# Kernel optimization log

Measured on AMD Instinct MI355X. Metric: run time of the kernel, lower is better.

The kernel has to match this reference:

```python
import jax, jax.numpy as jnp
import numpy as np

HID, INTER, DK = 768, 1536, 128
NEG_INF = 1.0e12
LOG512 = float(np.log(512.0))


def setup_inputs() -> dict:
    key = jax.random.key(0)
    k1, k2, k3 = jax.random.split(key, 3)
    B, S = 4, 2048
    hidden_states = jax.random.normal(k1, (B, S, HID), dtype=jnp.float32)
    attention_mask = jnp.ones((B, S), dtype=jnp.int32)
    # i_dense: hidden -> 2*INTER + DK (no bias); o_dense: INTER -> hidden (no bias)
    Wi = jax.random.normal(k2, (HID, 2 * INTER + DK), dtype=jnp.float32) * (HID ** -0.5)
    Wo = jax.random.normal(k3, (INTER, HID), dtype=jnp.float32) * (INTER ** -0.5)
    q_gamma = jnp.ones((DK,), dtype=jnp.float32)  # ScaleOffset scale, offset=False
    k_gamma = jnp.ones((DK,), dtype=jnp.float32)
    return {"hidden_states": hidden_states, "Wi": Wi, "Wo": Wo,
            "q_gamma": q_gamma, "k_gamma": k_gamma,
            "attention_mask": attention_mask}


def reference(hidden_states, Wi, Wo, q_gamma, k_gamma, attention_mask):
    # i_dense + swish, then split into u, v, qk
    x = jax.nn.silu(jnp.einsum('bsh,ho->bso', hidden_states, Wi))
    u = x[..., :INTER]
    v = x[..., INTER:2 * INTER]
    qk = x[..., 2 * INTER:]
    q = qk * q_gamma
    k = qk * k_gamma
    # single-head attention scores
    a = jnp.einsum('bmd,bnd->bmn', q, k) / (DK ** 0.5)
    mask = attention_mask[:, None, :]  # [B,1,N]
    a = jnp.where(mask == 0, -NEG_INF, a)
    l = jnp.sum(attention_mask, axis=-1, keepdims=True)[:, :, None].astype(a.dtype)  # [B,1,1]
    # softmax_plus: softmax(a * log(l) / log(512))
    A = jax.nn.softmax(a * jnp.log(l) / LOG512, axis=-1)
    # dropout inactive in eval mode
    o = jnp.einsum('bmi,ih->bmh', u * jnp.einsum('bmn,bnd->bmd', A, v), Wo)
    return o
```

## Files before the change

### kernel.cpp

```cpp
#include <hip/hip_runtime.h>
#include <hip/hip_bf16.h>
#include <math.h>

#define BATCH 4
#define SEQ   2048
#define HID   768
#define INTER 1536
#define DK    128
#define NTOT  3200
#define NTOTP 3328
#define MROWS 8192
#define LN512 6.2383246250395075f

typedef _Float16 half8   __attribute__((ext_vector_type(8)));
typedef _Float16 half4   __attribute__((ext_vector_type(4)));
typedef float    floatx4 __attribute__((ext_vector_type(4)));
typedef float    floatx16 __attribute__((ext_vector_type(16)));

typedef const __attribute__((address_space(1))) unsigned int* gas1_t;
typedef __attribute__((address_space(3))) unsigned int* las3_t;

static __device__ __forceinline__ void load16(const _Float16* g, _Float16* l) {
    __builtin_amdgcn_global_load_lds((gas1_t)g, (las3_t)l, 16, 0, 0);
}
#define WAIT_VM(N)    asm volatile("s_waitcnt vmcnt(" #N ")" ::: "memory")
#define WAIT_LGKM0()  asm volatile("s_waitcnt lgkmcnt(0)" ::: "memory")
#define BARRIER_RAW() asm volatile("s_barrier" ::: "memory")

__global__ __launch_bounds__(256) void prep_kernel(
    const float* __restrict__ H, _Float16* __restrict__ Hb,
    const float* __restrict__ Wi, _Float16* __restrict__ WiT,
    const float* __restrict__ Wo, _Float16* __restrict__ WoT,
    const int* __restrict__ mask, float* __restrict__ scales)
{
    __shared__ _Float16 tile[32][33];
    __shared__ int sh[256];
    const int bid = blockIdx.x, tid = threadIdx.x;
    if (bid < 3072) {
        const int i = (bid * 256 + tid) * 8;
        float4 a = *reinterpret_cast<const float4*>(H + i);
        float4 b = *reinterpret_cast<const float4*>(H + i + 4);
        half8 h = {(_Float16)a.x, (_Float16)a.y, (_Float16)a.z, (_Float16)a.w,
                   (_Float16)b.x, (_Float16)b.y, (_Float16)b.z, (_Float16)b.w};
        *reinterpret_cast<half8*>(Hb + i) = h;
    } else if (bid < 3072 + 2496) {
        const int l = bid - 3072;
        const int c0 = (l % 104) * 32, r0 = (l / 104) * 32;
        const int tx = tid & 31, ty = tid >> 5;
#pragma unroll
        for (int j = 0; j < 32; j += 8)
            tile[tx][ty + j] = (c0 + tx < NTOT)
                ? (_Float16)Wi[(size_t)(r0 + ty + j) * NTOT + c0 + tx]
                : (_Float16)0.0f;
        __syncthreads();
#pragma unroll
        for (int j = 0; j < 32; j += 8)
            WiT[(size_t)(c0 + ty + j) * HID + r0 + tx] = tile[ty + j][tx];
    } else if (bid < 3072 + 2496 + 1152) {
        const int l = bid - (3072 + 2496);
        const int c0 = (l % 24) * 32, r0 = (l / 24) * 32;
        const int tx = tid & 31, ty = tid >> 5;
#pragma unroll
        for (int j = 0; j < 32; j += 8)
            tile[tx][ty + j] = (_Float16)Wo[(size_t)(r0 + ty + j) * HID + c0 + tx];
        __syncthreads();
#pragma unroll
        for (int j = 0; j < 32; j += 8)
            WoT[(size_t)(c0 + ty + j) * INTER + r0 + tx] = tile[ty + j][tx];
    } else {
        const int b = bid - (3072 + 2496 + 1152);
        int s = 0;
        for (int i = tid; i < SEQ; i += 256) s += mask[b * SEQ + i];
        sh[tid] = s;
        __syncthreads();
        for (int off = 128; off > 0; off >>= 1) {
            if (tid < off) sh[tid] += sh[tid + off];
            __syncthreads();
        }
        if (tid == 0) scales[b] = logf((float)sh[0]) / LN512;
    }
}

struct TileCtx {
    int tid, wave, lane, quad, l16, l31, half, wm, wn, c0, c1;
};
static __device__ __forceinline__ TileCtx make_ctx() {
    TileCtx t;
    t.tid = threadIdx.x;
    t.wave = t.tid >> 6; t.lane = t.tid & 63;
    t.quad = t.lane >> 4; t.l16 = t.lane & 15;
    t.l31 = t.lane & 31;  t.half = t.lane >> 5;
    t.wm = (t.wave & 1) * 64;
    t.wn = (t.wave >> 1) * 64;
    t.c0 = t.tid;
    t.c1 = t.tid + 256;
    return t;
}

static __device__ __forceinline__ void gemm_mainloop_3s32(
    const TileCtx& t,
    const _Float16* __restrict__ Ag, int lda,
    const _Float16* __restrict__ Bg, int ldb,
    int K, _Float16* smem, floatx16 acc[2][2])
{
    const int r0i = t.c0 >> 2, s0 = (((r0i >> 1) ^ (r0i >> 3)) & 3);
    const int r1i = t.c1 >> 2, s1 = (((r1i >> 1) ^ (r1i >> 3)) & 3);
    const int ak0 = ((t.c0 & 3) ^ s0) * 8;
    const int ak1 = ((t.c1 & 3) ^ s1) * 8;
    const _Float16* a0 = Ag + (size_t)r0i * lda + ak0;
    const _Float16* a1 = Ag + (size_t)r1i * lda + ak1;
    const _Float16* b0 = Bg + (size_t)r0i * ldb + ak0;
    const _Float16* b1 = Bg + (size_t)r1i * ldb + ak1;
    _Float16* Asl = smem + t.c0 * 8;
    _Float16* Bsl = smem + 12288 + t.c0 * 8;
    const int nIter = K >> 5;

    const int fsw = ((t.l31 >> 1) ^ (t.l31 >> 3)) & 3;

    load16(a0, Asl);        load16(a1, Asl + 2048);
    load16(b0, Bsl);        load16(b1, Bsl + 2048);
    if (nIter > 1) {
        load16(a0 + 32, Asl + 4096); load16(a1 + 32, Asl + 6144);
        load16(b0 + 32, Bsl + 4096); load16(b1 + 32, Bsl + 6144);
    }

    int sc = 0, sp = 2;
    for (int k = 0; k < nIter; ++k) {
        if (k + 1 < nIter) { WAIT_VM(4); } else { WAIT_VM(0); }
        BARRIER_RAW();
        if (k + 2 < nIter) {
            const int off = sp * 4096;
            const int k0 = (k + 2) << 5;
            load16(a0 + k0, Asl + off); load16(a1 + k0, Asl + off + 2048);
            load16(b0 + k0, Bsl + off); load16(b1 + k0, Bsl + off + 2048);
        }
        const _Float16* Ab = smem + sc * 4096;
        const _Float16* Bb = smem + 12288 + sc * 4096;
        half8 af[2][2], bf[2][2];
#pragma unroll
        for (int mt = 0; mt < 2; ++mt)
#pragma unroll
            for (int h = 0; h < 2; ++h)
                af[mt][h] = *reinterpret_cast<const half8*>(
                    Ab + (t.wm + mt * 32 + t.l31) * 32 + (((h * 2 + t.half) ^ fsw) * 8));
#pragma unroll
        for (int nt = 0; nt < 2; ++nt)
#pragma unroll
            for (int h = 0; h < 2; ++h)
                bf[nt][h] = *reinterpret_cast<const half8*>(
                    Bb + (t.wn + nt * 32 + t.l31) * 32 + (((h * 2 + t.half) ^ fsw) * 8));
#pragma unroll
        for (int h = 0; h < 2; ++h)
#pragma unroll
            for (int mt = 0; mt < 2; ++mt)
#pragma unroll
                for (int nt = 0; nt < 2; ++nt)
                    acc[mt][nt] = __builtin_amdgcn_mfma_f32_32x32x16_f16(af[mt][h], bf[nt][h], acc[mt][nt], 0, 0, 0);
        WAIT_LGKM0();
        sc = (sc == 2) ? 0 : sc + 1;
        sp = (sp == 2) ? 0 : sp + 1;
    }
}

__global__ __launch_bounds__(512, 2) void gemm1_kernel(
    const _Float16* __restrict__ Hb, const _Float16* __restrict__ WiT,
    const float* __restrict__ qg, const float* __restrict__ kg,
    _Float16* __restrict__ u, _Float16* __restrict__ vT,
    _Float16* __restrict__ q, _Float16* __restrict__ k)
{
    __shared__ _Float16 smem[65536];
    const int tid = threadIdx.x;
    const int lane = tid & 63, wave = tid >> 6;
    const int quad = lane >> 4, l16 = lane & 15;
    const int wm = wave >> 2, wn = wave & 3;

    const int f = blockIdx.x;
    const int xcd = f & 7, i = f >> 3;
    const int m0 = (xcd * 4 + (i & 3)) * 256;
    const int ntile = i >> 2;
    const int n0 = ntile * 256;

    const _Float16* Ag = Hb  + (size_t)m0 * HID;
    const _Float16* Bg = WiT + (size_t)n0 * HID;

    const int rA = tid >> 2;
    const int csw = ((tid & 3) ^ ((rA >> 1) & 3)) * 8;
    const _Float16* pa0 = Ag + (size_t)rA * HID + csw;
    const _Float16* pa1 = pa0 + (size_t)128 * HID;
    const _Float16* pb0 = Bg + (size_t)rA * HID + csw;
    const _Float16* pb1 = pb0 + (size_t)128 * HID;

    const int sw8 = (l16 >> 1) & 3;
    const int qs  = (quad ^ sw8) * 8;
    const int aoff = (wm * 128 + l16) * 32 + qs;
    const int boff = 8192 + (wn * 64 + l16) * 32 + qs;

    floatx4 acc[8][4] = {};

    const int nKt = HID / 32;

#pragma unroll
    for (int pt = 0; pt < 3; ++pt) {
        _Float16* ld = smem + pt * 16384 + tid * 8;
        const int ko = pt * 32;
        load16(pa0 + ko, ld);
        load16(pa1 + ko, ld + 4096);
        load16(pb0 + ko, ld + 8192);
        load16(pb1 + ko, ld + 12288);
    }
    WAIT_VM(8);
    BARRIER_RAW();

    for (int t = 0; t < nKt; ++t) {
        const _Float16* sl = smem + (t & 3) * 16384;
        if (t + 3 < nKt) {
            _Float16* ld = smem + ((t + 3) & 3) * 16384 + tid * 8;
            const int ko = (t + 3) * 32;
            load16(pa0 + ko, ld);        load16(pa1 + ko, ld + 4096);
            load16(pb0 + ko, ld + 8192); load16(pb1 + ko, ld + 12288);
        }
        half8 af[8], bf[4];
#pragma unroll
        for (int mt = 0; mt < 8; ++mt)
            af[mt] = *reinterpret_cast<const half8*>(sl + aoff + mt * 512);
#pragma unroll
        for (int nt = 0; nt < 4; ++nt)
            bf[nt] = *reinterpret_cast<const half8*>(sl + boff + nt * 512);
        __builtin_amdgcn_s_setprio(1);
#pragma unroll
        for (int mt = 0; mt < 8; ++mt)
#pragma unroll
            for (int nt = 0; nt < 4; ++nt)
                acc[mt][nt] = __builtin_amdgcn_mfma_f32_16x16x32_f16(af[mt], bf[nt], acc[mt][nt], 0, 0, 0);
        __builtin_amdgcn_s_setprio(0);
        if (t <= nKt - 4)      { WAIT_VM(8); }
        else if (t == nKt - 3) { WAIT_VM(4); }
        else if (t == nKt - 2) { WAIT_VM(0); }
        BARRIER_RAW();
    }
    __syncthreads();

    if (ntile < 6) {
#pragma unroll
        for (int mt = 0; mt < 8; ++mt) {
#pragma unroll
            for (int nt = 0; nt < 4; ++nt) {
                const int col = n0 + wn * 64 + nt * 16 + l16;
#pragma unroll
                for (int i2 = 0; i2 < 4; ++i2) {
                    const int row = m0 + wm * 128 + mt * 16 + quad * 4 + i2;
                    float x = acc[mt][nt][i2];
                    float y = x / (1.0f + __expf(-x));
                    u[(size_t)row * INTER + col] = (_Float16)y;
                }
            }
        }
    } else if (ntile < 12) {
        const int bb = m0 >> 11, sloc = m0 & (SEQ - 1), cI = n0 - INTER;
#pragma unroll
        for (int mt = 0; mt < 8; ++mt) {
#pragma unroll
            for (int nt = 0; nt < 4; ++nt) {
                const int cl  = wn * 64 + nt * 16 + l16;
                const int rl0 = wm * 128 + mt * 16 + quad * 4;
                half4 pk;
#pragma unroll
                for (int i2 = 0; i2 < 4; ++i2) {
                    float x = acc[mt][nt][i2];
                    pk[i2] = (_Float16)(x / (1.0f + __expf(-x)));
                }
                *reinterpret_cast<half4*>(smem + cl * 256 + (rl0 ^ ((cl & 31) << 3))) = pk;
            }
        }
        __syncthreads();
#pragma unroll
        for (int p = 0; p < 16; ++p) {
            const int chunk = p * 512 + tid;
            const int cl = chunk >> 5, scn = chunk & 31;
            half8 v = *reinterpret_cast<const half8*>(smem + cl * 256 + ((scn ^ (cl & 31)) << 3));
            *reinterpret_cast<half8*>(vT + ((size_t)bb * INTER + cI + cl) * SEQ + sloc + scn * 8) = v;
        }
    } else {
        if (wn < 2) {
#pragma unroll
            for (int mt = 0; mt < 8; ++mt) {
#pragma unroll
                for (int nt = 0; nt < 4; ++nt) {
                    const int cq = wn * 64 + nt * 16 + l16;
                    const float qgv = qg[cq], kgv = kg[cq];
#pragma unroll
                    for (int i2 = 0; i2 < 4; ++i2) {
                        const int row = m0 + wm * 128 + mt * 16 + quad * 4 + i2;
                        float x = acc[mt][nt][i2];
                        float y = x / (1.0f + __expf(-x));
                        q[(size_t)row * DK + cq] = (_Float16)(y * qgv);
                        k[(size_t)row * DK + cq] = (_Float16)(y * kgv);
                    }
                }
            }
        }
    }
}

__global__ __launch_bounds__(256) void scores_kernel(
    const _Float16* __restrict__ q, const _Float16* __restrict__ k,
    const int* __restrict__ mask, const float* __restrict__ scales,
    _Float16* __restrict__ P)
{
    __shared__ _Float16 ps[16 * 2056];
    __shared__ float redmax[4][16];
    __shared__ float redsum[4][16];
    const int f = blockIdx.x;
    const int xcd = f & 7, i = f >> 3;
    const int b = xcd >> 1;
    const int m0 = ((xcd & 1) * 64 + i) * 16;
    const int tid = threadIdx.x;
    const int wave = tid >> 6, lane = tid & 63, quad = lane >> 4, l16 = lane & 15;
    const float scale = scales[b];

    half8 aq[4];
    const _Float16* qrow = q + (b * SEQ + m0 + l16) * DK + quad * 8;
#pragma unroll
    for (int kk = 0; kk < 4; ++kk) aq[kk] = *reinterpret_cast<const half8*>(qrow + kk * 32);

    floatx4 sc[32];
#pragma unroll
    for (int nt = 0; nt < 32; ++nt) {
        int n0 = nt * 64 + wave * 16;
        const _Float16* krow = k + (b * SEQ + n0 + l16) * DK + quad * 8;
        floatx4 acc = {};
#pragma unroll
        for (int kk = 0; kk < 4; ++kk) {
            half8 bq = *reinterpret_cast<const half8*>(krow + kk * 32);
            acc = __builtin_amdgcn_mfma_f32_16x16x32_f16(aq[kk], bq, acc, 0, 0, 0);
        }
        sc[nt] = acc;
    }

    const float rs = 0.08838834764831845f * scale;
    const float mval = -1e12f * scale;
    float rmax[4] = {-3.4e38f, -3.4e38f, -3.4e38f, -3.4e38f};
#pragma unroll
    for (int nt = 0; nt < 32; ++nt) {
        int ncol = nt * 64 + wave * 16 + l16;
        bool mok = mask[b * SEQ + ncol] != 0;
#pragma unroll
        for (int i2 = 0; i2 < 4; ++i2) {
            float s = mok ? sc[nt][i2] * rs : mval;
            sc[nt][i2] = s;
            rmax[i2] = fmaxf(rmax[i2], s);
        }
    }
#pragma unroll
    for (int i2 = 0; i2 < 4; ++i2) {
#pragma unroll
        for (int off = 1; off < 16; off <<= 1)
            rmax[i2] = fmaxf(rmax[i2], __shfl_xor(rmax[i2], off, 64));
    }
    if (l16 == 0) {
#pragma unroll
        for (int i2 = 0; i2 < 4; ++i2) redmax[wave][quad * 4 + i2] = rmax[i2];
    }
    __syncthreads();
#pragma unroll
    for (int i2 = 0; i2 < 4; ++i2) {
        int r = quad * 4 + i2;
        rmax[i2] = fmaxf(fmaxf(redmax[0][r], redmax[1][r]), fmaxf(redmax[2][r], redmax[3][r]));
    }
    float rsum[4] = {0.f, 0.f, 0.f, 0.f};
#pragma unroll
    for (int nt = 0; nt < 32; ++nt) {
#pragma unroll
        for (int i2 = 0; i2 < 4; ++i2) {
            float e = __expf(sc[nt][i2] - rmax[i2]);
            sc[nt][i2] = e;
            rsum[i2] += e;
        }
    }
#pragma unroll
    for (int i2 = 0; i2 < 4; ++i2) {
#pragma unroll
        for (int off = 1; off < 16; off <<= 1) rsum[i2] += __shfl_xor(rsum[i2], off, 64);
    }
    if (l16 == 0) {
#pragma unroll
        for (int i2 = 0; i2 < 4; ++i2) redsum[wave][quad * 4 + i2] = rsum[i2];
    }
    __syncthreads();
#pragma unroll
    for (int i2 = 0; i2 < 4; ++i2) {
        int r = quad * 4 + i2;
        float tot = redsum[0][r] + redsum[1][r] + redsum[2][r] + redsum[3][r];
        float inv = 1.0f / tot;
#pragma unroll
        for (int nt = 0; nt < 32; ++nt) {
            int ncol = nt * 64 + wave * 16 + l16;
            ps[r * 2056 + ncol] = (_Float16)(sc[nt][i2] * inv);
        }
    }
    __syncthreads();
    _Float16* Pb = P + ((size_t)b * SEQ + m0) * SEQ;
#pragma unroll
    for (int p = 0; p < 16; ++p) {
        const int chunk = p * 256 + tid;
        const int row = chunk >> 8, c8 = chunk & 255;
        half8 v = *reinterpret_cast<const half8*>(ps + row * 2056 + c8 * 8);
        *reinterpret_cast<half8*>(Pb + (size_t)row * SEQ + c8 * 8) = v;
    }
}

__global__ __launch_bounds__(256) void pv_kernel(
    const _Float16* __restrict__ P, const _Float16* __restrict__ vT,
    _Float16* __restrict__ u)
{
    __shared__ _Float16 smem[24576];
    TileCtx t = make_ctx();
    const int f = blockIdx.x;
    const int xcd = f & 7, i = f >> 3;
    const int b = i / 24, j = i % 24;
    const int m0 = (xcd * 2 + (j & 1)) * 128;
    const int n0 = (j >> 1) * 128;
    const _Float16* Pb  = P  + (size_t)b * SEQ * SEQ;
    const _Float16* vTb = vT + (size_t)b * INTER * SEQ;

    floatx16 acc[2][2] = {};
    gemm_mainloop_3s32(t, Pb + (size_t)m0 * SEQ, SEQ, vTb + (size_t)n0 * SEQ, SEQ, SEQ, smem, acc);

#pragma unroll
    for (int mt = 0; mt < 2; ++mt) {
#pragma unroll
        for (int nt = 0; nt < 2; ++nt) {
            int col = n0 + t.wn + nt * 32 + t.l31;
#pragma unroll
            for (int reg = 0; reg < 16; ++reg) {
                int row = m0 + t.wm + mt * 32 + (reg & 3) + 8 * (reg >> 2) + 4 * t.half;
                size_t gidx = ((size_t)(b * SEQ + row)) * INTER + col;
                float uv = (float)u[gidx];
                u[gidx] = (_Float16)(acc[mt][nt][reg] * uv);
            }
        }
    }
}

__global__ __launch_bounds__(256) void gemm2_kernel(
    const _Float16* __restrict__ tin, const _Float16* __restrict__ WoT,
    float* __restrict__ out)
{
    __shared__ _Float16 smem[24576];
    TileCtx t = make_ctx();
    const int f = blockIdx.x;
    const int xcd = f & 7, i = f >> 3;
    const int m0 = ((xcd << 3) | (i & 7)) * 128;
    const int n0 = (i >> 3) * 128;

    floatx16 acc[2][2] = {};
    gemm_mainloop_3s32(t, tin + (size_t)m0 * INTER, INTER, WoT + (size_t)n0 * INTER, INTER, INTER, smem, acc);

#pragma unroll
    for (int mt = 0; mt < 2; ++mt) {
#pragma unroll
        for (int nt = 0; nt < 2; ++nt) {
            int col = n0 + t.wn + nt * 32 + t.l31;
#pragma unroll
            for (int reg = 0; reg < 16; ++reg) {
                int row = m0 + t.wm + mt * 32 + (reg & 3) + 8 * (reg >> 2) + 4 * t.half;
                out[(size_t)row * HID + col] = acc[mt][nt][reg];
            }
        }
    }
}

extern "C" void kernel_launch(void* const* d_in, const int* in_sizes, int n_in,
                              void* d_out, int out_size, void* d_ws, size_t ws_size,
                              hipStream_t stream) {
    const float* H    = (const float*)d_in[0];
    const float* Wi   = (const float*)d_in[1];
    const float* Wo   = (const float*)d_in[2];
    const float* qg   = (const float*)d_in[3];
    const float* kg   = (const float*)d_in[4];
    const int*   mask = (const int*)d_in[5];
    float* out = (float*)d_out;

    char* base = (char*)d_ws;
    size_t off = 0;
    auto alloc = [&](size_t bytes) { void* p = base + off; off = (off + bytes + 255) & ~(size_t)255; return p; };
    _Float16* Hb   = (_Float16*)alloc((size_t)MROWS * HID * 2);
    _Float16* WiT  = (_Float16*)alloc((size_t)NTOTP * HID * 2);
    _Float16* WoT  = (_Float16*)alloc((size_t)HID * INTER * 2);
    _Float16* u    = (_Float16*)alloc((size_t)MROWS * INTER * 2);
    _Float16* vT   = (_Float16*)alloc((size_t)BATCH * INTER * SEQ * 2);
    _Float16* q    = (_Float16*)alloc((size_t)MROWS * DK * 2);
    _Float16* k    = (_Float16*)alloc((size_t)MROWS * DK * 2);
    _Float16* P    = (_Float16*)alloc((size_t)BATCH * SEQ * SEQ * 2);
    float*    scales = (float*)alloc(4 * sizeof(float));

    prep_kernel<<<6724, 256, 0, stream>>>(H, Hb, Wi, WiT, Wo, WoT, mask, scales);
    gemm1_kernel<<<416, 512, 0, stream>>>(Hb, WiT, qg, kg, u, vT, q, k);
    scores_kernel<<<512, 256, 0, stream>>>(q, k, mask, scales, P);
    pv_kernel<<<768, 256, 0, stream>>>(P, vT, u);
    gemm2_kernel<<<384, 256, 0, stream>>>(u, WoT, out);
}
```

Before: 296.5 us.

## Store P in fragment-ordered layout and stream A fragments directly to registers in PV

The softmax kernel now writes P in a blocked layout with 8-element column chunks interleaved across rows, so each MFMA A-fragment is one contiguous 16-byte global load. The PV kernel loads its P operand straight into registers with double-buffered fragments and keeps only the V^T tile in LDS with a 3-stage ring, which halves shared memory. This removes the LDS staging and LDS reads for the P operand, at the cost of hand-tuned vmcnt waits and more register pressure. The global reads of P are also less coalesced across rows.

Measured after the change: 293.1 us. Within noise of the previous version (-1.1%).

```diff
diff --git a/kernel.cpp b/kernel.cpp
--- a/kernel.cpp
+++ b/kernel.cpp
@@ -26,6 +26,8 @@
 #define WAIT_VM(N)    asm volatile("s_waitcnt vmcnt(" #N ")" ::: "memory")
 #define WAIT_LGKM0()  asm volatile("s_waitcnt lgkmcnt(0)" ::: "memory")
 #define BARRIER_RAW() asm volatile("s_barrier" ::: "memory")
+#define GLOAD16(dst, ptr) \
+    asm volatile("global_load_dwordx4 %0, %1, off" : "=v"(dst) : "v"(ptr) : "memory")
 
 __global__ __launch_bounds__(256) void prep_kernel(
     const float* __restrict__ H, _Float16* __restrict__ Hb,
@@ -399,32 +401,101 @@
         }
     }
     __syncthreads();
-    _Float16* Pb = P + ((size_t)b * SEQ + m0) * SEQ;
+    _Float16* Pfb = P + (size_t)b * SEQ * SEQ;
 #pragma unroll
     for (int p = 0; p < 16; ++p) {
         const int chunk = p * 256 + tid;
-        const int row = chunk >> 8, c8 = chunk & 255;
+        const int row = chunk & 15, c8 = chunk >> 4;
         half8 v = *reinterpret_cast<const half8*>(ps + row * 2056 + c8 * 8);
-        *reinterpret_cast<half8*>(Pb + (size_t)row * SEQ + c8 * 8) = v;
-    }
+        *reinterpret_cast<half8*>(Pfb + ((size_t)c8 * SEQ + m0 + row) * 8) = v;
+    }
+}
+
+static __device__ __forceinline__ void pv_iter(
+    const TileCtx& t, int k, _Float16* smem,
+    const _Float16* b0, const _Float16* b1,
+    const _Float16* pA0, const _Float16* pA1,
+    half8 (&afc)[2][2], half8 (&afn)[2][2],
+    floatx16 acc[2][2], int fsw)
+{
+    const _Float16* Bb = smem + (k % 3) * 4096;
+    half8 bf[2][2];
+#pragma unroll
+    for (int nt = 0; nt < 2; ++nt)
+#pragma unroll
+        for (int h = 0; h < 2; ++h)
+            bf[nt][h] = *reinterpret_cast<const half8*>(
+                Bb + (t.wn + nt * 32 + t.l31) * 32 + (((h * 2 + t.half) ^ fsw) * 8));
+    if (k + 1 < 64) {
+        const size_t co = (size_t)(k + 1) * 4 * (SEQ * 8);
+        GLOAD16(afn[0][0], pA0 + co);
+        GLOAD16(afn[0][1], pA0 + co + 2 * (SEQ * 8));
+        GLOAD16(afn[1][0], pA1 + co);
+        GLOAD16(afn[1][1], pA1 + co + 2 * (SEQ * 8));
+    }
+    if (k + 2 < 64) {
+        _Float16* ld = smem + ((k + 2) % 3) * 4096 + t.c0 * 8;
+        const int ko = (k + 2) * 32;
+        load16(b0 + ko, ld);
+        load16(b1 + ko, ld + 2048);
+    }
+    if (k <= 61)      { WAIT_VM(6); }
+    else if (k == 62) { WAIT_VM(4); }
+    else              { WAIT_VM(0); }
+    __builtin_amdgcn_sched_barrier(0);
+    __builtin_amdgcn_s_setprio(1);
+#pragma unroll
+    for (int h = 0; h < 2; ++h)
+#pragma unroll
+        for (int mt = 0; mt < 2; ++mt)
+#pragma unroll
+            for (int nt = 0; nt < 2; ++nt)
+                acc[mt][nt] = __builtin_amdgcn_mfma_f32_32x32x16_f16(afc[mt][h], bf[nt][h], acc[mt][nt], 0, 0, 0);
+    __builtin_amdgcn_s_setprio(0);
+    BARRIER_RAW();
 }
 
 __global__ __launch_bounds__(256) void pv_kernel(
-    const _Float16* __restrict__ P, const _Float16* __restrict__ vT,
+    const _Float16* __restrict__ Pf, const _Float16* __restrict__ vT,
     _Float16* __restrict__ u)
 {
-    __shared__ _Float16 smem[24576];
+    __shared__ _Float16 smem[12288];
     TileCtx t = make_ctx();
     const int f = blockIdx.x;
     const int xcd = f & 7, i = f >> 3;
     const int b = i / 24, j = i % 24;
     const int m0 = (xcd * 2 + (j & 1)) * 128;
     const int n0 = (j >> 1) * 128;
-    const _Float16* Pb  = P  + (size_t)b * SEQ * SEQ;
+    const _Float16* Pfb = Pf + (size_t)b * SEQ * SEQ;
     const _Float16* vTb = vT + (size_t)b * INTER * SEQ;
 
+    const int r0i = t.c0 >> 2, s0 = (((r0i >> 1) ^ (r0i >> 3)) & 3);
+    const int r1i = t.c1 >> 2, s1 = (((r1i >> 1) ^ (r1i >> 3)) & 3);
+    const _Float16* b0 = vTb + (size_t)(n0 + r0i) * SEQ + ((t.c0 & 3) ^ s0) * 8;
+    const _Float16* b1 = vTb + (size_t)(n0 + r1i) * SEQ + ((t.c1 & 3) ^ s1) * 8;
+    _Float16* Bsl = smem + t.c0 * 8;
+    const int fsw = ((t.l31 >> 1) ^ (t.l31 >> 3)) & 3;
+
+    const _Float16* pA0 = Pfb + (size_t)t.half * (SEQ * 8)
+                        + (size_t)(m0 + t.wm + t.l31) * 8;
+    const _Float16* pA1 = pA0 + 32 * 8;
+
     floatx16 acc[2][2] = {};
-    gemm_mainloop_3s32(t, Pb + (size_t)m0 * SEQ, SEQ, vTb + (size_t)n0 * SEQ, SEQ, SEQ, smem, acc);
+    half8 afA[2][2], afB[2][2];
+
+    load16(b0, Bsl);        load16(b1, Bsl + 2048);
+    load16(b0 + 32, Bsl + 4096); load16(b1 + 32, Bsl + 6144);
+    GLOAD16(afA[0][0], pA0);
+    GLOAD16(afA[0][1], pA0 + 2 * (SEQ * 8));
+    GLOAD16(afA[1][0], pA1);
+    GLOAD16(afA[1][1], pA1 + 2 * (SEQ * 8));
+    WAIT_VM(4);
+    BARRIER_RAW();
+
+    for (int k = 0; k < 64; k += 2) {
+        pv_iter(t, k,     smem, b0, b1, pA0, pA1, afA, afB, acc, fsw);
+        pv_iter(t, k + 1, smem, b0, b1, pA0, pA1, afB, afA, acc, fsw);
+    }
 
 #pragma unroll
     for (int mt = 0; mt < 2; ++mt) {
```

## Register double-buffer fragments across GEMMs and load P directly in MFMA layout

Applied to the files above, without the earlier changes.

Reworks the GEMM main loops in gemm1, gemm2 and pv so LDS fragment reads for the next k-step are issued before the MFMAs of the current step, with ping-pong register buffers, a 4-slot LDS ring, and one barrier per iteration. The softmax kernel now writes P in a fragment-friendly interleaved layout ([k/8][row][8]). This lets pv_kernel read its A operand straight from global memory into registers via inline global_load_dwordx4, skipping LDS for P. The goal is to hide LDS latency and cut barrier and LDS traffic. The cost is higher register pressure and hand-tuned vmcnt waits, which could break if the load counts change.

Result: no change. 298.0 us (+0.5%).

```diff
diff --git a/kernel.cpp b/kernel.cpp
--- a/kernel.cpp
+++ b/kernel.cpp
@@ -26,6 +26,8 @@
 #define WAIT_VM(N)    asm volatile("s_waitcnt vmcnt(" #N ")" ::: "memory")
 #define WAIT_LGKM0()  asm volatile("s_waitcnt lgkmcnt(0)" ::: "memory")
 #define BARRIER_RAW() asm volatile("s_barrier" ::: "memory")
+#define GLOAD16(dst, ptr) \
+    asm volatile("global_load_dwordx4 %0, %1, off" : "=v"(dst) : "v"(ptr) : "memory")
 
 __global__ __launch_bounds__(256) void prep_kernel(
     const float* __restrict__ H, _Float16* __restrict__ Hb,
@@ -97,7 +99,56 @@
     return t;
 }
 
-static __device__ __forceinline__ void gemm_mainloop_3s32(
+#define RO32_READ(FR, SLOT) do {                                               \
+    const _Float16* Ab_ = smem + (SLOT) * 8192;                                \
+    const _Float16* Bb_ = Ab_ + 4096;                                          \
+    _Pragma("unroll")                                                          \
+    for (int mt = 0; mt < 2; ++mt)                                             \
+        _Pragma("unroll")                                                      \
+        for (int h = 0; h < 2; ++h)                                            \
+            FR##a[mt][h] = *reinterpret_cast<const half8*>(                    \
+                Ab_ + (t.wm + mt * 32 + t.l31) * 32 + (((h * 2 + t.half) ^ fsw) * 8)); \
+    _Pragma("unroll")                                                          \
+    for (int nt = 0; nt < 2; ++nt)                                             \
+        _Pragma("unroll")                                                      \
+        for (int h = 0; h < 2; ++h)                                            \
+            FR##b[nt][h] = *reinterpret_cast<const half8*>(                    \
+                Bb_ + (t.wn + nt * 32 + t.l31) * 32 + (((h * 2 + t.half) ^ fsw) * 8)); \
+} while (0)
+
+#define RO32_MMA(FR) do {                                                      \
+    __builtin_amdgcn_s_setprio(1);                                             \
+    _Pragma("unroll")                                                          \
+    for (int h = 0; h < 2; ++h)                                                \
+        _Pragma("unroll")                                                      \
+        for (int mt = 0; mt < 2; ++mt)                                         \
+            _Pragma("unroll")                                                  \
+            for (int nt = 0; nt < 2; ++nt)                                     \
+                acc[mt][nt] = __builtin_amdgcn_mfma_f32_32x32x16_f16(          \
+                    FR##a[mt][h], FR##b[nt][h], acc[mt][nt], 0, 0, 0);         \
+    __builtin_amdgcn_s_setprio(0);                                             \
+} while (0)
+
+#define RO32_STAGE(K) do {                                                     \
+    _Float16* ld_ = smem2 + ((K) & 3) * 8192 + t.c0 * 8;                       \
+    const int ko_ = (K) << 5;                                                  \
+    load16(a0 + ko_, ld_);        load16(a1 + ko_, ld_ + 2048);                \
+    load16(b0 + ko_, ld_ + 4096); load16(b1 + ko_, ld_ + 6144);                \
+} while (0)
+
+#define RO32_ITER(K, CUR, NXT) do {                                            \
+    if ((K) + 2 < nIter) RO32_STAGE((K) + 2);                                  \
+    if ((K) + 2 < nIter)      { WAIT_VM(4); }                                  \
+    else if ((K) + 1 < nIter) { WAIT_VM(0); }                                  \
+    else                      { WAIT_VM(0); }                                  \
+    __builtin_amdgcn_sched_barrier(0);                                         \
+    BARRIER_RAW();                                                             \
+    if ((K) + 1 < nIter) RO32_READ(NXT, ((K) + 1) & 3);                        \
+    RO32_MMA(CUR);                                                             \
+    WAIT_LGKM0();                                                              \
+} while (0)
+
+static __device__ __forceinline__ void gemm_mainloop_ro32(
     const TileCtx& t,
     const _Float16* __restrict__ Ag, int lda,
     const _Float16* __restrict__ Bg, int ldb,
@@ -105,60 +156,25 @@
 {
     const int r0i = t.c0 >> 2, s0 = (((r0i >> 1) ^ (r0i >> 3)) & 3);
     const int r1i = t.c1 >> 2, s1 = (((r1i >> 1) ^ (r1i >> 3)) & 3);
-    const int ak0 = ((t.c0 & 3) ^ s0) * 8;
-    const int ak1 = ((t.c1 & 3) ^ s1) * 8;
-    const _Float16* a0 = Ag + (size_t)r0i * lda + ak0;
-    const _Float16* a1 = Ag + (size_t)r1i * lda + ak1;
-    const _Float16* b0 = Bg + (size_t)r0i * ldb + ak0;
-    const _Float16* b1 = Bg + (size_t)r1i * ldb + ak1;
-    _Float16* Asl = smem + t.c0 * 8;
-    _Float16* Bsl = smem + 12288 + t.c0 * 8;
+    const _Float16* a0 = Ag + (size_t)r0i * lda + ((t.c0 & 3) ^ s0) * 8;
+    const _Float16* a1 = Ag + (size_t)r1i * lda + ((t.c1 & 3) ^ s1) * 8;
+    const _Float16* b0 = Bg + (size_t)r0i * ldb + ((t.c0 & 3) ^ s0) * 8;
+    const _Float16* b1 = Bg + (size_t)r1i * ldb + ((t.c1 & 3) ^ s1) * 8;
+    _Float16* smem2 = smem;
     const int nIter = K >> 5;
-
     const int fsw = ((t.l31 >> 1) ^ (t.l31 >> 3)) & 3;
 
-    load16(a0, Asl);        load16(a1, Asl + 2048);
-    load16(b0, Bsl);        load16(b1, Bsl + 2048);
-    if (nIter > 1) {
-        load16(a0 + 32, Asl + 4096); load16(a1 + 32, Asl + 6144);
-        load16(b0 + 32, Bsl + 4096); load16(b1 + 32, Bsl + 6144);
-    }
-
-    int sc = 0, sp = 2;
-    for (int k = 0; k < nIter; ++k) {
-        if (k + 1 < nIter) { WAIT_VM(4); } else { WAIT_VM(0); }
-        BARRIER_RAW();
-        if (k + 2 < nIter) {
-            const int off = sp * 4096;
-            const int k0 = (k + 2) << 5;
-            load16(a0 + k0, Asl + off); load16(a1 + k0, Asl + off + 2048);
-            load16(b0 + k0, Bsl + off); load16(b1 + k0, Bsl + off + 2048);
-        }
-        const _Float16* Ab = smem + sc * 4096;
-        const _Float16* Bb = smem + 12288 + sc * 4096;
-        half8 af[2][2], bf[2][2];
-#pragma unroll
-        for (int mt = 0; mt < 2; ++mt)
-#pragma unroll
-            for (int h = 0; h < 2; ++h)
-                af[mt][h] = *reinterpret_cast<const half8*>(
-                    Ab + (t.wm + mt * 32 + t.l31) * 32 + (((h * 2 + t.half) ^ fsw) * 8));
-#pragma unroll
-        for (int nt = 0; nt < 2; ++nt)
-#pragma unroll
-            for (int h = 0; h < 2; ++h)
-                bf[nt][h] = *reinterpret_cast<const half8*>(
-                    Bb + (t.wn + nt * 32 + t.l31) * 32 + (((h * 2 + t.half) ^ fsw) * 8));
-#pragma unroll
-        for (int h = 0; h < 2; ++h)
-#pragma unroll
-            for (int mt = 0; mt < 2; ++mt)
-#pragma unroll
-                for (int nt = 0; nt < 2; ++nt)
-                    acc[mt][nt] = __builtin_amdgcn_mfma_f32_32x32x16_f16(af[mt][h], bf[nt][h], acc[mt][nt], 0, 0, 0);
-        WAIT_LGKM0();
-        sc = (sc == 2) ? 0 : sc + 1;
-        sp = (sp == 2) ? 0 : sp + 1;
+    half8 pa[2][2], pb[2][2], qa[2][2], qb[2][2];
+
+    RO32_STAGE(0);
+    RO32_STAGE(1);
+    WAIT_VM(4);
+    BARRIER_RAW();
+    RO32_READ(p, 0);
+
+    for (int k = 0; k < nIter; k += 2) {
+        RO32_ITER(k,     p, q);
+        RO32_ITER(k + 1, q, p);
     }
 }
 
@@ -196,47 +212,54 @@
     const int boff = 8192 + (wn * 64 + l16) * 32 + qs;
 
     floatx4 acc[8][4] = {};
+    half8 pa_[8], pb_[4], qa_[8], qb_[4];
 
     const int nKt = HID / 32;
 
-#pragma unroll
-    for (int pt = 0; pt < 3; ++pt) {
-        _Float16* ld = smem + pt * 16384 + tid * 8;
-        const int ko = pt * 32;
-        load16(pa0 + ko, ld);
-        load16(pa1 + ko, ld + 4096);
-        load16(pb0 + ko, ld + 8192);
-        load16(pb1 + ko, ld + 12288);
-    }
+#define G1_STAGE(T) do {                                                       \
+        _Float16* ld_ = smem + ((T) & 3) * 16384 + tid * 8;                    \
+        const int ko_ = (T) << 5;                                              \
+        load16(pa0 + ko_, ld_);        load16(pa1 + ko_, ld_ + 4096);          \
+        load16(pb0 + ko_, ld_ + 8192); load16(pb1 + ko_, ld_ + 12288);         \
+    } while (0)
+
+#define G1_READ(AF, BF, SLOT) do {                                             \
+        const _Float16* sl_ = smem + (SLOT) * 16384;                           \
+        _Pragma("unroll")                                                      \
+        for (int mt = 0; mt < 8; ++mt)                                         \
+            AF[mt] = *reinterpret_cast<const half8*>(sl_ + aoff + mt * 512);   \
+        _Pragma("unroll")                                                      \
+        for (int nt = 0; nt < 4; ++nt)                                         \
+            BF[nt] = *reinterpret_cast<const half8*>(sl_ + boff + nt * 512);   \
+    } while (0)
+
+#define G1_ITER(T, AFC, BFC, AFN, BFN) do {                                    \
+        if ((T) + 3 < nKt) G1_STAGE((T) + 3);                                  \
+        if ((T) + 3 < nKt)      { WAIT_VM(8); }                                \
+        else if ((T) + 2 < nKt) { WAIT_VM(4); }                                \
+        else                    { WAIT_VM(0); }                                \
+        __builtin_amdgcn_sched_barrier(0);                                     \
+        BARRIER_RAW();                                                         \
+        if ((T) + 1 < nKt) G1_READ(AFN, BFN, ((T) + 1) & 3);                   \
+        __builtin_amdgcn_s_setprio(1);                                         \
+        _Pragma("unroll")                                                      \
+        for (int mt = 0; mt < 8; ++mt)                                         \
+            _Pragma("unroll")                                                  \
+            for (int nt = 0; nt < 4; ++nt)                                     \
+                acc[mt][nt] = __builtin_amdgcn_mfma_f32_16x16x32_f16(          \
+                    AFC[mt], BFC[nt], acc[mt][nt], 0, 0, 0);                   \
+        __builtin_amdgcn_s_setprio(0);                                         \
+        WAIT_LGKM0();                                                          \
+    } while (0)
+
+    G1_STAGE(0); G1_STAGE(1); G1_STAGE(2);
     WAIT_VM(8);
     BARRIER_RAW();
-
-    for (int t = 0; t < nKt; ++t) {
-        const _Float16* sl = smem + (t & 3) * 16384;
-        if (t + 3 < nKt) {
-            _Float16* ld = smem + ((t + 3) & 3) * 16384 + tid * 8;
-            const int ko = (t + 3) * 32;
-            load16(pa0 + ko, ld);        load16(pa1 + ko, ld + 4096);
-            load16(pb0 + ko, ld + 8192); load16(pb1 + ko, ld + 12288);
-        }
-        half8 af[8], bf[4];
-#pragma unroll
-        for (int mt = 0; mt < 8; ++mt)
-            af[mt] = *reinterpret_cast<const half8*>(sl + aoff + mt * 512);
-#pragma unroll
-        for (int nt = 0; nt < 4; ++nt)
-            bf[nt] = *reinterpret_cast<const half8*>(sl + boff + nt * 512);
-        __builtin_amdgcn_s_setprio(1);
-#pragma unroll
-        for (int mt = 0; mt < 8; ++mt)
-#pragma unroll
-            for (int nt = 0; nt < 4; ++nt)
-                acc[mt][nt] = __builtin_amdgcn_mfma_f32_16x16x32_f16(af[mt], bf[nt], acc[mt][nt], 0, 0, 0);
-        __builtin_amdgcn_s_setprio(0);
-        if (t <= nKt - 4)      { WAIT_VM(8); }
-        else if (t == nKt - 3) { WAIT_VM(4); }
-        else if (t == nKt - 2) { WAIT_VM(0); }
-        BARRIER_RAW();
+    G1_READ(pa_, pb_, 0);
+
+    for (int t = 0; t < nKt; t += 2) {
+        G1_ITER(t,     pa_, pb_, qa_, qb_);
+        G1_ITER(t + 1, qa_, qb_, pa_, pb_);
     }
     __syncthreads();
 
@@ -399,32 +422,101 @@
         }
     }
     __syncthreads();
-    _Float16* Pb = P + ((size_t)b * SEQ + m0) * SEQ;
+    _Float16* Pfb = P + (size_t)b * SEQ * SEQ;
 #pragma unroll
     for (int p = 0; p < 16; ++p) {
         const int chunk = p * 256 + tid;
-        const int row = chunk >> 8, c8 = chunk & 255;
+        const int row = chunk & 15, c8 = chunk >> 4;
         half8 v = *reinterpret_cast<const half8*>(ps + row * 2056 + c8 * 8);
-        *reinterpret_cast<half8*>(Pb + (size_t)row * SEQ + c8 * 8) = v;
+        *reinterpret_cast<half8*>(Pfb + ((size_t)c8 * SEQ + m0 + row) * 8) = v;
     }
 }
 
 __global__ __launch_bounds__(256) void pv_kernel(
-    const _Float16* __restrict__ P, const _Float16* __restrict__ vT,
+    const _Float16* __restrict__ Pf, const _Float16* __restrict__ vT,
     _Float16* __restrict__ u)
 {
-    __shared__ _Float16 smem[24576];
+    __shared__ _Float16 smem[16384];
     TileCtx t = make_ctx();
     const int f = blockIdx.x;
     const int xcd = f & 7, i = f >> 3;
     const int b = i / 24, j = i % 24;
     const int m0 = (xcd * 2 + (j & 1)) * 128;
     const int n0 = (j >> 1) * 128;
-    const _Float16* Pb  = P  + (size_t)b * SEQ * SEQ;
+    const _Float16* Pfb = Pf + (size_t)b * SEQ * SEQ;
     const _Float16* vTb = vT + (size_t)b * INTER * SEQ;
 
+    const int r0i = t.c0 >> 2, s0 = (((r0i >> 1) ^ (r0i >> 3)) & 3);
+    const int r1i = t.c1 >> 2, s1 = (((r1i >> 1) ^ (r1i >> 3)) & 3);
+    const _Float16* b0 = vTb + (size_t)(n0 + r0i) * SEQ + ((t.c0 & 3) ^ s0) * 8;
+    const _Float16* b1 = vTb + (size_t)(n0 + r1i) * SEQ + ((t.c1 & 3) ^ s1) * 8;
+    const int fsw = ((t.l31 >> 1) ^ (t.l31 >> 3)) & 3;
+
+    const _Float16* pA0 = Pfb + (size_t)t.half * (SEQ * 8)
+                        + (size_t)(m0 + t.wm + t.l31) * 8;
+    const _Float16* pA1 = pA0 + 32 * 8;
+
     floatx16 acc[2][2] = {};
-    gemm_mainloop_3s32(t, Pb + (size_t)m0 * SEQ, SEQ, vTb + (size_t)n0 * SEQ, SEQ, SEQ, smem, acc);
+    half8 afA[2][2], afB[2][2], bfA[2][2], bfB[2][2];
+
+#define PV_GLOADA(AF, K) do {                                                  \
+        const size_t co_ = (size_t)(K) * 4 * (SEQ * 8);                        \
+        GLOAD16(AF[0][0], pA0 + co_);                                          \
+        GLOAD16(AF[0][1], pA0 + co_ + 2 * (SEQ * 8));                          \
+        GLOAD16(AF[1][0], pA1 + co_);                                          \
+        GLOAD16(AF[1][1], pA1 + co_ + 2 * (SEQ * 8));                          \
+    } while (0)
+
+#define PV_STAGEB(K) do {                                                      \
+        _Float16* ld_ = smem + ((K) & 3) * 4096 + t.c0 * 8;                    \
+        const int ko_ = (K) << 5;                                              \
+        load16(b0 + ko_, ld_);                                                 \
+        load16(b1 + ko_, ld_ + 2048);                                          \
+    } while (0)
+
+#define PV_READB(BF, SLOT) do {                                                \
+        const _Float16* Bb_ = smem + (SLOT) * 4096;                            \
+        _Pragma("unroll")                                                      \
+        for (int nt = 0; nt < 2; ++nt)                                         \
+            _Pragma("unroll")                                                  \
+            for (int h = 0; h < 2; ++h)                                        \
+                BF[nt][h] = *reinterpret_cast<const half8*>(                   \
+                    Bb_ + (t.wn + nt * 32 + t.l31) * 32 + (((h * 2 + t.half) ^ fsw) * 8)); \
+    } while (0)
+
+#define PV_ITER(K, AFC, BFC, AFN, BFN) do {                                    \
+        if ((K) + 1 < 64) PV_GLOADA(AFN, (K) + 1);                             \
+        if ((K) + 2 < 64) PV_STAGEB((K) + 2);                                  \
+        if ((K) + 2 < 64)      { WAIT_VM(6); }                                 \
+        else if ((K) + 1 < 64) { WAIT_VM(4); }                                 \
+        else                   { WAIT_VM(0); }                                 \
+        __builtin_amdgcn_sched_barrier(0);                                     \
+        BARRIER_RAW();                                                         \
+        if ((K) + 1 < 64) PV_READB(BFN, ((K) + 1) & 3);                        \
+        __builtin_amdgcn_s_setprio(1);                                         \
+        _Pragma("unroll")                                                      \
+        for (int h = 0; h < 2; ++h)                                            \
+            _Pragma("unroll")                                                  \
+            for (int mt = 0; mt < 2; ++mt)                                     \
+                _Pragma("unroll")                                              \
+                for (int nt = 0; nt < 2; ++nt)                                 \
+                    acc[mt][nt] = __builtin_amdgcn_mfma_f32_32x32x16_f16(      \
+                        AFC[mt][h], BFC[nt][h], acc[mt][nt], 0, 0, 0);         \
+        __builtin_amdgcn_s_setprio(0);                                         \
+        WAIT_LGKM0();                                                          \
+    } while (0)
+
+    PV_STAGEB(0);
+    PV_STAGEB(1);
+    PV_GLOADA(afA, 0);
+    WAIT_VM(6);
+    BARRIER_RAW();
+    PV_READB(bfA, 0);
+
+    for (int k = 0; k < 64; k += 2) {
+        PV_ITER(k,     afA, bfA, afB, bfB);
+        PV_ITER(k + 1, afB, bfB, afA, bfA);
+    }
 
 #pragma unroll
     for (int mt = 0; mt < 2; ++mt) {
@@ -446,7 +538,7 @@
     const _Float16* __restrict__ tin, const _Float16* __restrict__ WoT,
     float* __restrict__ out)
 {
-    __shared__ _Float16 smem[24576];
+    __shared__ _Float16 smem[32768];
     TileCtx t = make_ctx();
     const int f = blockIdx.x;
     const int xcd = f & 7, i = f >> 3;
@@ -454,7 +546,7 @@
     const int n0 = (i >> 3) * 128;
 
     floatx16 acc[2][2] = {};
-    gemm_mainloop_3s32(t, tin + (size_t)m0 * INTER, INTER, WoT + (size_t)n0 * INTER, INTER, INTER, smem, acc);
+    gemm_mainloop_ro32(t, tin + (size_t)m0 * INTER, INTER, WoT + (size_t)n0 * INTER, INTER, INTER, smem, acc);
 
 #pragma unroll
     for (int mt = 0; mt < 2; ++mt) {
```
